# Kernel optimization log

Measured on AMD Instinct MI355X. Metric: run time of the kernel, lower is better.

The kernel has to match this reference:

```python
import jax, jax.numpy as jnp
import numpy as np

N, E, IN, H, OUT, L = 20000, 320000, 256, 256, 128, 3
EPS = 1e-5


def setup_inputs() -> dict:
    key = jax.random.key(0)
    ks = jax.random.split(key, 16)
    s = 0.02
    return {
        "x": jax.random.normal(ks[0], (N, IN), jnp.float32),
        "edge_index": jax.random.randint(ks[1], (2, E), 0, N, jnp.int64),
        "in_w": jax.random.normal(ks[2], (IN, H), jnp.float32) * s,
        "in_b": jnp.zeros((H,), jnp.float32),
        "parent_w": jax.random.normal(ks[3], (L, H, H), jnp.float32) * s,
        "child_w": jax.random.normal(ks[4], (L, H, H), jnp.float32) * s,
        "self_w": jax.random.normal(ks[5], (L, H, H), jnp.float32) * s,
        "self_b": jnp.zeros((L, H), jnp.float32),
        "ln_g": jnp.ones((L, H), jnp.float32),
        "ln_b": jnp.zeros((L, H), jnp.float32),
        "head_w1": jax.random.normal(ks[6], (H, H), jnp.float32) * s,
        "head_b1": jnp.zeros((H,), jnp.float32),
        "head_w2": jax.random.normal(ks[7], (H, OUT), jnp.float32) * s,
        "head_b2": jnp.zeros((OUT,), jnp.float32),
    }


def _aggregate(h, src, dst, weight):
    # gather -> matmul -> scatter-add -> degree-normalize
    transformed = h[src] @ weight                       # [E, H]
    agg = jax.ops.segment_sum(transformed, dst, num_segments=N)
    deg = jax.ops.segment_sum(jnp.ones((src.shape[0],), h.dtype), dst, num_segments=N)
    deg = jnp.maximum(deg, 1.0)
    return agg / deg[:, None]


def _layer_norm(x, g, b):
    mu = jnp.mean(x, axis=-1, keepdims=True)
    var = jnp.mean(jnp.square(x - mu), axis=-1, keepdims=True)
    return (x - mu) * jax.lax.rsqrt(var + EPS) * g + b


def reference(x, edge_index, in_w, in_b, parent_w, child_w, self_w, self_b,
              ln_g, ln_b, head_w1, head_b1, head_w2, head_b2):
    src, dst = edge_index[0], edge_index[1]
    h = x @ in_w + in_b                                  # input_proj
    for l in range(L):
        parent_msg = _aggregate(h, src, dst, parent_w[l])
        child_msg = _aggregate(h, dst, src, child_w[l])  # reversed edges
        out = h @ self_w[l] + self_b[l] + parent_msg + child_msg
        out = jax.nn.gelu(out, approximate=False)
        # dropout is identity in eval mode (training=False)
        h = _layer_norm(h + out, ln_g[l], ln_b[l])
    y = jax.nn.gelu(h @ head_w1 + head_b1, approximate=False)
    return y @ head_w2 + head_b2
```

## Files before the change

### kernel.cpp

```cpp
#include <hip/hip_runtime.h>


#define H 256
#define LAYERS 3
#define OUTD 128
#define LN_EPS 1e-5f

typedef short s16x8 __attribute__((ext_vector_type(8)));
typedef unsigned short u16x4 __attribute__((ext_vector_type(4)));
typedef unsigned short u16x8 __attribute__((ext_vector_type(8)));
typedef float f32x4 __attribute__((ext_vector_type(4)));
typedef int i32x4 __attribute__((ext_vector_type(4)));

__device__ __forceinline__ unsigned short f2bf(float f) {
  unsigned int u = __float_as_uint(f);
  u += 0x7FFFu + ((u >> 16) & 1u);
  return (unsigned short)(u >> 16);
}
__device__ __forceinline__ float bf2f(unsigned short s) {
  return __uint_as_float(((unsigned int)s) << 16);
}
__device__ __forceinline__ float gelu_f(float x) {
  return 0.5f * x * (1.0f + erff(x * 0.70710678118654752440f));
}
__device__ __forceinline__ void gload16(const void* g, void* l) {
  __builtin_amdgcn_global_load_lds((const __attribute__((address_space(1))) void*)g,
                                   (__attribute__((address_space(3))) void*)l, 16, 0, 0);
}


__device__ __forceinline__ void store_split8(unsigned short* __restrict__ T, int NS, int sec,
                                             int row, int l, u16x4 hv, u16x4 lv) {
  size_t tb = ((size_t)((row >> 4) * NS + sec) << 4) + (l >> 3);
  int off = (((row & 15) + (((l >> 1) & 3) << 4)) << 3) + ((l & 1) << 2);
  *(u16x4*)(T + tb * 512 + off) = hv;
  *(u16x4*)(T + (tb + 8) * 512 + off) = lv;
}

__global__ void split_tiles_kernel(const float* __restrict__ X,
                                   unsigned short* __restrict__ T, int NS, int sec,
                                   unsigned short* __restrict__ Hc, int M)
{
  const int rb = blockIdx.x;
  const int l = threadIdx.x & 63;
  const int cq = threadIdx.x >> 6;
  const int row = (rb << 4) + (l & 15);
  if (row >= M) return;
  const float* xr = X + (size_t)row * H;
#pragma unroll
  for (int p = 0; p < 2; ++p) {
    const int c = cq + (p << 2);
    const int j0 = (c << 5) + ((l >> 4) << 3);
    f32x4 v0 = *(const f32x4*)(xr + j0);
    f32x4 v1 = *(const f32x4*)(xr + j0 + 4);
    u16x8 hv, lv;
#pragma unroll
    for (int i = 0; i < 4; ++i) {
      unsigned short hb = f2bf(v0[i]); hv[i] = hb;     lv[i] = f2bf(v0[i] - bf2f(hb));
      unsigned short hc = f2bf(v1[i]); hv[4 + i] = hc; lv[4 + i] = f2bf(v1[i] - bf2f(hc));
    }
    size_t tb = ((size_t)(rb * NS + sec) << 4);
    *(u16x8*)(T + (tb + c) * 512 + (l << 3)) = hv;
    *(u16x8*)(T + (tb + c + 8) * 512 + (l << 3)) = lv;
    if (Hc) *(u16x8*)(Hc + (size_t)row * H + j0) = hv;
  }
}

__global__ void bext_kernel(const float* __restrict__ W, unsigned short* __restrict__ Bt, int ncol) {
  int idx = blockIdx.x * 256 + threadIdx.x;
  if (idx >= H * ncol) return;
  int k = idx / ncol;
  int n = idx - k * ncol;
  float w = W[idx];
  unsigned short hb = f2bf(w);
  unsigned short lb = f2bf(w - bf2f(hb));
  size_t base = (((size_t)(n >> 4) << 4) + (k >> 5)) * 512 +
                (((n & 15) + (((k >> 3) & 3) << 4)) << 3) + (k & 7);
  Bt[base] = hb;
  Bt[base + 8 * 512] = lb;
}

__global__ void zero2_kernel(int* __restrict__ a, int* __restrict__ b, int n) {
  int i = blockIdx.x * 256 + threadIdx.x;
  if (i < n) { a[i] = 0; b[i] = 0; }
}

__global__ void deg_kernel(const int* __restrict__ src, const int* __restrict__ dst,
                           int* __restrict__ di, int* __restrict__ dox, int E) {
  int e = blockIdx.x * 256 + threadIdx.x;
  if (e >= E) return;
  atomicAdd(&dox[src[e]], 1);
  atomicAdd(&di[dst[e]], 1);
}

__global__ void rdeg_kernel(const int* __restrict__ di, const int* __restrict__ dox,
                            float* __restrict__ ri, float* __restrict__ ro, int n) {
  int i = blockIdx.x * 256 + threadIdx.x;
  if (i >= n) return;
  int a = di[i];  if (a < 1) a = 1;
  int b = dox[i]; if (b < 1) b = 1;
  ri[i] = 1.0f / (float)a;
  ro[i] = 1.0f / (float)b;
}

__global__ __launch_bounds__(1024)
void scan_kernel(const int* __restrict__ deg, int* __restrict__ rowptr, int n) {
  __shared__ int partial[1024];
  const int t = threadIdx.x;
  const int chunk = (n + 1023) / 1024;
  int b = t * chunk;
  int e = b + chunk; if (e > n) e = n;
  int s = 0;
  for (int i = b; i < e; ++i) s += deg[i];
  partial[t] = s;
  __syncthreads();
  for (int off = 1; off < 1024; off <<= 1) {
    int v = (t >= off) ? partial[t - off] : 0;
    __syncthreads();
    partial[t] += v;
    __syncthreads();
  }
  int run = (t == 0) ? 0 : partial[t - 1];
  for (int i = b; i < e; ++i) { rowptr[i] = run; run += deg[i]; }
  if (t == 1023) rowptr[n] = run;
}

__global__ void fill_kernel(const int* __restrict__ src, const int* __restrict__ dst,
                            const int* __restrict__ rp_in, const int* __restrict__ rp_out,
                            int* __restrict__ cur_in, int* __restrict__ cur_out,
                            int* __restrict__ ci_in, int* __restrict__ ci_out, int E) {
  int e = blockIdx.x * 256 + threadIdx.x;
  if (e >= E) return;
  int s = src[e], d = dst[e];
  int p = atomicAdd(&cur_in[d], 1);
  ci_in[rp_in[d] + p] = s;
  int q = atomicAdd(&cur_out[s], 1);
  ci_out[rp_out[s] + q] = d;
}

template<int NF>
__global__ __launch_bounds__(256)
void gemm_kernel(const unsigned short* __restrict__ A, int NSa,
                 const unsigned short* __restrict__ B0,
                 const unsigned short* __restrict__ B1,
                 const unsigned short* __restrict__ B2,
                 const float* __restrict__ bias, float* __restrict__ C,
                 int M, int nrb, int nsec, int do_gelu)
{
  constexpr int N = NF * 64;
  constexpr int NBT = N / 16;
  constexpr int BITER = NBT / 4;
  constexpr int SA_HI = 0, SA_LO = 2048, SB_HI = 4096;
  constexpr int SB_LO = 4096 + NBT * 512;
  __shared__ unsigned short lds[2][4096 + 2 * NBT * 512];

  const int tid = threadIdx.x;
  const int lane = tid & 63;
  const int wn = tid >> 6;
  const int m0 = blockIdx.x << 6;
  int rbw = (blockIdx.x << 2) + wn;
  if (rbw >= nrb) rbw = nrb - 1;

  f32x4 acc[4][NF] = {};

  auto STAGE = [&](int buf, int step) {
    const int s = step >> 3;
    const int c = step & 7;
    const unsigned short* Bs = (s == 0) ? B0 : ((s == 1) ? B1 : B2);
    unsigned short* base = &lds[buf][0];
    const unsigned short* pa = A + (((size_t)(rbw * NSa + s) << 4) + c) * 512 + (lane << 3);
    gload16(pa,        base + SA_HI + (wn << 9));
    gload16(pa + 4096, base + SA_LO + (wn << 9));
#pragma unroll
    for (int i = 0; i < BITER; ++i) {
      const int nb = wn + (i << 2);
      const unsigned short* pb = Bs + (((size_t)nb << 4) + c) * 512 + (lane << 3);
      gload16(pb,        base + SB_HI + (nb << 9));
      gload16(pb + 4096, base + SB_LO + (nb << 9));
    }
  };

  auto COMPUTE = [&](int buf) {
    const unsigned short* base = &lds[buf][0];
    s16x8 ah[4], al[4], bh[NF], bl[NF];
#pragma unroll
    for (int f = 0; f < 4; ++f) {
      ah[f] = *(const s16x8*)(base + SA_HI + (f << 9) + (lane << 3));
      al[f] = *(const s16x8*)(base + SA_LO + (f << 9) + (lane << 3));
    }
#pragma unroll
    for (int j = 0; j < NF; ++j) {
      const int g = wn * NF + j;
      bh[j] = *(const s16x8*)(base + SB_HI + (g << 9) + (lane << 3));
      bl[j] = *(const s16x8*)(base + SB_LO + (g << 9) + (lane << 3));
    }
#pragma unroll
    for (int i = 0; i < 4; ++i)
#pragma unroll
      for (int j = 0; j < NF; ++j)
        acc[i][j] = __builtin_amdgcn_mfma_f32_16x16x32_bf16(ah[i], bh[j], acc[i][j], 0, 0, 0);
#pragma unroll
    for (int i = 0; i < 4; ++i)
#pragma unroll
      for (int j = 0; j < NF; ++j)
        acc[i][j] = __builtin_amdgcn_mfma_f32_16x16x32_bf16(ah[i], bl[j], acc[i][j], 0, 0, 0);
#pragma unroll
    for (int i = 0; i < 4; ++i)
#pragma unroll
      for (int j = 0; j < NF; ++j)
        acc[i][j] = __builtin_amdgcn_mfma_f32_16x16x32_bf16(al[i], bh[j], acc[i][j], 0, 0, 0);
  };

  const int nsteps = nsec << 3;
  STAGE(0, 0);
  int cur = 0;
  for (int t = 0; t < nsteps - 1; ++t) {
    STAGE(cur ^ 1, t + 1);
    if (NF == 4) asm volatile("s_waitcnt vmcnt(10)" ::: "memory");
    else         asm volatile("s_waitcnt vmcnt(6)"  ::: "memory");
    __builtin_amdgcn_s_barrier();
    COMPUTE(cur);
    asm volatile("s_waitcnt lgkmcnt(0)" ::: "memory");
    __builtin_amdgcn_s_barrier();
    cur ^= 1;
  }
  asm volatile("s_waitcnt vmcnt(0)" ::: "memory");
  __builtin_amdgcn_s_barrier();
  COMPUTE(cur);

  const int r0 = (lane >> 4) << 2;
  const int cn = lane & 15;
#pragma unroll
  for (int j = 0; j < NF; ++j) {
    const int col = wn * (NF << 4) + (j << 4) + cn;
    const float bb = bias ? bias[col] : 0.0f;
#pragma unroll
    for (int i = 0; i < 4; ++i) {
      const int rowb = m0 + (i << 4) + r0;
#pragma unroll
      for (int r = 0; r < 4; ++r) {
        const int rr = rowb + r;
        if (rr < M) {
          float v = acc[i][j][r] + bb;
          if (do_gelu) v = gelu_f(v);
          C[(size_t)rr * N + col] = v;
        }
      }
    }
  }
}

__device__ __forceinline__ void gacc8(const int* __restrict__ ci, int beg, int end,
                                      const unsigned short* __restrict__ Hc, int foff,
                                      float* __restrict__ acc) {
  int i = beg;
  for (; i < end && (i & 3); ++i) {
    u16x8 a = *(const u16x8*)(Hc + ((size_t)ci[i] << 8) + foff);
#pragma unroll
    for (int z = 0; z < 8; ++z) acc[z] += bf2f(a[z]);
  }
  for (; i + 4 <= end; i += 4) {
    i32x4 id = *(const i32x4*)(ci + i);
    u16x8 a = *(const u16x8*)(Hc + ((size_t)id[0] << 8) + foff);
    u16x8 b = *(const u16x8*)(Hc + ((size_t)id[1] << 8) + foff);
    u16x8 c = *(const u16x8*)(Hc + ((size_t)id[2] << 8) + foff);
    u16x8 d = *(const u16x8*)(Hc + ((size_t)id[3] << 8) + foff);
#pragma unroll
    for (int z = 0; z < 8; ++z)
      acc[z] += (bf2f(a[z]) + bf2f(b[z])) + (bf2f(c[z]) + bf2f(d[z]));
  }
  for (; i < end; ++i) {
    u16x8 a = *(const u16x8*)(Hc + ((size_t)ci[i] << 8) + foff);
#pragma unroll
    for (int z = 0; z < 8; ++z) acc[z] += bf2f(a[z]);
  }
}

__global__ __launch_bounds__(256)
void gather_kernel(
    const int* __restrict__ rp_in, const int* __restrict__ ci_in,
    const int* __restrict__ rp_out, const int* __restrict__ ci_out,
    const float* __restrict__ ri, const float* __restrict__ ro,
    const unsigned short* __restrict__ Hc, unsigned short* __restrict__ Aext,
    int M, int nrb, int npair)
{
  __shared__ unsigned short sh[2][2][2][2][512];
  const int b = blockIdx.x;
  const int xcd = b & 7;
  const int s = xcd >> 1;
  const int rbp = ((b >> 3) << 1) + (xcd & 1);
  if (rbp >= npair) return;
  const int tid = threadIdx.x;
  const int g = tid >> 3;
  const int t = tid & 7;
  const int row = (rbp << 5) + g;
  const int foff = (s << 6) + (t << 3);

  float hin[8] = {}, hout[8] = {};
  float wi = 0.f, wo = 0.f;
  if (row < M) {
    gacc8(ci_in,  rp_in[row],  rp_in[row + 1],  Hc, foff, hin);
    gacc8(ci_out, rp_out[row], rp_out[row + 1], Hc, foff, hout);
    wi = ri[row];
    wo = ro[row];
  }

  const int rbl = g >> 4;
  const int cc = t >> 2;
  const int pos = ((g & 15) << 3) + ((t & 3) << 7);
  u16x8 hv, lv;
#pragma unroll
  for (int q = 0; q < 8; ++q) {
    float v = hin[q] * wi;
    unsigned short hb = f2bf(v);
    hv[q] = hb; lv[q] = f2bf(v - bf2f(hb));
  }
  *(u16x8*)(&sh[rbl][0][0][cc][pos]) = hv;
  *(u16x8*)(&sh[rbl][0][1][cc][pos]) = lv;
#pragma unroll
  for (int q = 0; q < 8; ++q) {
    float v = hout[q] * wo;
    unsigned short hb = f2bf(v);
    hv[q] = hb; lv[q] = f2bf(v - bf2f(hb));
  }
  *(u16x8*)(&sh[rbl][1][0][cc][pos]) = hv;
  *(u16x8*)(&sh[rbl][1][1][cc][pos]) = lv;
  __syncthreads();

  const int tp = tid >> 4;
  const int q = tid & 15;
  const int rbl2 = tp >> 3, sec = (tp >> 2) & 1, hilo = (tp >> 1) & 1, c2 = tp & 1;
  const int rb = (rbp << 1) + rbl2;
  if (rb < nrb) {
    const int cg = (s << 1) + c2 + (hilo << 3);
    size_t tile = ((size_t)(rb * 3 + 1 + sec) << 4) + cg;
    unsigned short* dstp = Aext + tile * 512;
    const unsigned short* srcp = &sh[rbl2][sec][hilo][c2][0];
#pragma unroll
    for (int i = 0; i < 4; ++i)
      *(u16x8*)(dstp + (i << 7) + (q << 3)) = *(const u16x8*)(srcp + (i << 7) + (q << 3));
  }
}

__global__ void finalize_kernel(float* __restrict__ h, const float* __restrict__ P,
                                unsigned short* __restrict__ Aext,
                                unsigned short* __restrict__ Hc,
                                const float* __restrict__ g, const float* __restrict__ b, int M)
{
  int row = blockIdx.x * 4 + (threadIdx.x >> 6);
  if (row >= M) return;
  int l = threadIdx.x & 63;
  int j = l << 2;
  f32x4 hv = *(const f32x4*)(h + (size_t)row * H + j);
  f32x4 pv = *(const f32x4*)(P + (size_t)row * H + j);
  f32x4 t;
  float sum = 0.f, sq = 0.f;
#pragma unroll
  for (int i = 0; i < 4; ++i) {
    t[i] = hv[i] + gelu_f(pv[i]);
    sum += t[i];
    sq += t[i] * t[i];
  }
#pragma unroll
  for (int off = 1; off < 64; off <<= 1) {
    sum += __shfl_xor(sum, off, 64);
    sq  += __shfl_xor(sq, off, 64);
  }
  float mu = sum * (1.0f / H);
  float var = sq * (1.0f / H) - mu * mu;
  float rs = rsqrtf(var + LN_EPS);
  f32x4 outv;
  u16x4 hvv, lvv;
#pragma unroll
  for (int i = 0; i < 4; ++i) {
    outv[i] = (t[i] - mu) * rs * g[j + i] + b[j + i];
    unsigned short hb = f2bf(outv[i]);
    hvv[i] = hb;
    lvv[i] = f2bf(outv[i] - bf2f(hb));
  }
  *(f32x4*)(h + (size_t)row * H + j) = outv;
  *(u16x4*)(Hc + ((size_t)row << 8) + j) = hvv;
  store_split8(Aext, 3, 0, row, l, hvv, lvv);
}

extern "C" void kernel_launch(void* const* d_in, const int* in_sizes, int n_in,
                              void* d_out, int out_size, void* d_ws, size_t ws_size,
                              hipStream_t stream)
{
  const float* x        = (const float*)d_in[0];
  const int*   ei       = (const int*)d_in[1];
  const float* in_w     = (const float*)d_in[2];
  const float* in_b     = (const float*)d_in[3];
  const float* parent_w = (const float*)d_in[4];
  const float* child_w  = (const float*)d_in[5];
  const float* self_w   = (const float*)d_in[6];
  const float* self_b   = (const float*)d_in[7];
  const float* ln_g     = (const float*)d_in[8];
  const float* ln_b     = (const float*)d_in[9];
  const float* head_w1  = (const float*)d_in[10];
  const float* head_b1  = (const float*)d_in[11];
  const float* head_w2  = (const float*)d_in[12];
  const float* head_b2  = (const float*)d_in[13];

  const int M = in_sizes[0] / H;
  const int E = in_sizes[1] / 2;
  const int nrb = (M + 15) / 16;
  const int npair = (nrb + 1) / 2;
  const int* src = ei;
  const int* dst = ei + E;

  char* w = (char*)d_ws;
  auto alloc = [&](size_t bytes) { char* p = w; w += (bytes + 255) & ~(size_t)255; return p; };
  float*          h    = (float*)alloc((size_t)M * H * 4);
  float*          P    = (float*)alloc((size_t)M * H * 4);
  unsigned short* Ax   = (unsigned short*)alloc((size_t)nrb * 16 * 512 * 2);
  unsigned short* Aext = (unsigned short*)alloc((size_t)nrb * 48 * 512 * 2);
  unsigned short* Hc   = (unsigned short*)alloc((size_t)M * H * 2);
  unsigned short* Bext = (unsigned short*)alloc((size_t)12 * H * 512 * 2);
  int*            degi = (int*)alloc((size_t)M * 4);
  int*            dego = (int*)alloc((size_t)M * 4);
  float*          ri   = (float*)alloc((size_t)M * 4);
  float*          ro   = (float*)alloc((size_t)M * 4);
  int*            rp_in   = (int*)alloc((size_t)(M + 1) * 4);
  int*            rp_out  = (int*)alloc((size_t)(M + 1) * 4);
  int*            cur_in  = (int*)alloc((size_t)M * 4);
  int*            cur_out = (int*)alloc((size_t)M * 4);
  int*            ci_in   = (int*)alloc((size_t)E * 4);
  int*            ci_out  = (int*)alloc((size_t)E * 4);
  if ((size_t)(w - (char*)d_ws) > ws_size) return;

  auto bslot = [&](int i) { return Bext + (size_t)i * H * 512; };

  bext_kernel<<<(H * H) / 256, 256, 0, stream>>>(in_w, bslot(0), H);
  for (int l = 0; l < LAYERS; ++l) {
    bext_kernel<<<(H * H) / 256, 256, 0, stream>>>(parent_w + (size_t)l * H * H, bslot(1 + l), H);
    bext_kernel<<<(H * H) / 256, 256, 0, stream>>>(child_w  + (size_t)l * H * H, bslot(4 + l), H);
    bext_kernel<<<(H * H) / 256, 256, 0, stream>>>(self_w   + (size_t)l * H * H, bslot(7 + l), H);
  }
  bext_kernel<<<(H * H) / 256, 256, 0, stream>>>(head_w1, bslot(10), H);
  bext_kernel<<<(H * OUTD) / 256, 256, 0, stream>>>(head_w2, bslot(11), OUTD);

  zero2_kernel<<<(M + 255) / 256, 256, 0, stream>>>(degi, dego, M);
  deg_kernel<<<(E + 255) / 256, 256, 0, stream>>>(src, dst, degi, dego, E);
  rdeg_kernel<<<(M + 255) / 256, 256, 0, stream>>>(degi, dego, ri, ro, M);
  scan_kernel<<<1, 1024, 0, stream>>>(degi, rp_in, M);
  scan_kernel<<<1, 1024, 0, stream>>>(dego, rp_out, M);
  zero2_kernel<<<(M + 255) / 256, 256, 0, stream>>>(cur_in, cur_out, M);
  fill_kernel<<<(E + 255) / 256, 256, 0, stream>>>(src, dst, rp_in, rp_out,
                                                   cur_in, cur_out, ci_in, ci_out, E);

  const int mb = (M + 63) / 64;
  const int ggrid = (M + 3) / 4;
  const int xgrid = 8 * ((npair + 1) / 2);

  split_tiles_kernel<<<nrb, 256, 0, stream>>>(x, Ax, 1, 0, nullptr, M);
  gemm_kernel<4><<<mb, 256, 0, stream>>>(Ax, 1, bslot(0), nullptr, nullptr,
                                         in_b, h, M, nrb, 1, 0);
  split_tiles_kernel<<<nrb, 256, 0, stream>>>(h, Aext, 3, 0, Hc, M);

  for (int l = 0; l < LAYERS; ++l) {
    gather_kernel<<<xgrid, 256, 0, stream>>>(rp_in, ci_in, rp_out, ci_out,
                                             ri, ro, Hc, Aext, M, nrb, npair);
    gemm_kernel<4><<<mb, 256, 0, stream>>>(Aext, 3,
                                           bslot(7 + l), bslot(1 + l), bslot(4 + l),
                                           self_b + (size_t)l * H, P, M, nrb, 3, 0);
    finalize_kernel<<<ggrid, 256, 0, stream>>>(h, P, Aext, Hc,
                                               ln_g + (size_t)l * H, ln_b + (size_t)l * H, M);
  }

  gemm_kernel<4><<<mb, 256, 0, stream>>>(Aext, 3, bslot(10), nullptr, nullptr,
                                         head_b1, P, M, nrb, 1, 1);
  split_tiles_kernel<<<nrb, 256, 0, stream>>>(P, Ax, 1, 0, nullptr, M);
  gemm_kernel<2><<<mb, 256, 0, stream>>>(Ax, 1, bslot(11), nullptr, nullptr,
                                         head_b2, (float*)d_out, M, nrb, 1, 0);
}
```

Measured before the change: 522.8 us.

## Batch weight-split and CSR-build launches, interleave in/out gather loops

Merges the eleven per-matrix weight-splitting launches into a single kernel indexed by slot. Folds the cursor zeroing into the reciprocal-degree kernel and runs both prefix scans as two blocks of one launch. The gather kernel now walks the in-edge and out-edge lists together, issuing eight independent row loads per iteration instead of processing the two lists one after the other. Together these cut launch count and raise memory-level parallelism in the gather, at the cost of more registers per thread there.

```diff
diff --git a/kernel.cpp b/kernel.cpp
--- a/kernel.cpp
+++ b/kernel.cpp
@@ -66,9 +66,26 @@
   }
 }
 
-__global__ void bext_kernel(const float* __restrict__ W, unsigned short* __restrict__ Bt, int ncol) {
-  int idx = blockIdx.x * 256 + threadIdx.x;
+__global__ void bext_all_kernel(const float* __restrict__ in_w,
+                                const float* __restrict__ parent_w,
+                                const float* __restrict__ child_w,
+                                const float* __restrict__ self_w,
+                                const float* __restrict__ head_w1,
+                                const float* __restrict__ head_w2,
+                                unsigned short* __restrict__ Bext)
+{
+  const int slot = blockIdx.x >> 8;
+  const int chunk = blockIdx.x & 255;
+  const int ncol = (slot == 11) ? OUTD : H;
+  const int idx = chunk * 256 + threadIdx.x;
   if (idx >= H * ncol) return;
+  const float* W =
+    (slot == 0)  ? in_w :
+    (slot <= 3)  ? parent_w + (size_t)(slot - 1) * H * H :
+    (slot <= 6)  ? child_w  + (size_t)(slot - 4) * H * H :
+    (slot <= 9)  ? self_w   + (size_t)(slot - 7) * H * H :
+    (slot == 10) ? head_w1  : head_w2;
+  unsigned short* Bt = Bext + (size_t)slot * H * 512;
   int k = idx / ncol;
   int n = idx - k * ncol;
   float w = W[idx];
@@ -94,18 +111,24 @@
 }
 
 __global__ void rdeg_kernel(const int* __restrict__ di, const int* __restrict__ dox,
-                            float* __restrict__ ri, float* __restrict__ ro, int n) {
+                            float* __restrict__ ri, float* __restrict__ ro,
+                            int* __restrict__ cur_in, int* __restrict__ cur_out, int n) {
   int i = blockIdx.x * 256 + threadIdx.x;
   if (i >= n) return;
   int a = di[i];  if (a < 1) a = 1;
   int b = dox[i]; if (b < 1) b = 1;
   ri[i] = 1.0f / (float)a;
   ro[i] = 1.0f / (float)b;
+  cur_in[i] = 0;
+  cur_out[i] = 0;
 }
 
 __global__ __launch_bounds__(1024)
-void scan_kernel(const int* __restrict__ deg, int* __restrict__ rowptr, int n) {
+void scan2_kernel(const int* __restrict__ degi, const int* __restrict__ dego,
+                  int* __restrict__ rp_in, int* __restrict__ rp_out, int n) {
   __shared__ int partial[1024];
+  const int* deg = blockIdx.x ? dego : degi;
+  int* rowptr = blockIdx.x ? rp_out : rp_in;
   const int t = threadIdx.x;
   const int chunk = (n + 1023) / 1024;
   int b = t * chunk;
@@ -250,30 +273,9 @@
   }
 }
 
-__device__ __forceinline__ void gacc8(const int* __restrict__ ci, int beg, int end,
-                                      const unsigned short* __restrict__ Hc, int foff,
-                                      float* __restrict__ acc) {
-  int i = beg;
-  for (; i < end && (i & 3); ++i) {
-    u16x8 a = *(const u16x8*)(Hc + ((size_t)ci[i] << 8) + foff);
-#pragma unroll
-    for (int z = 0; z < 8; ++z) acc[z] += bf2f(a[z]);
-  }
-  for (; i + 4 <= end; i += 4) {
-    i32x4 id = *(const i32x4*)(ci + i);
-    u16x8 a = *(const u16x8*)(Hc + ((size_t)id[0] << 8) + foff);
-    u16x8 b = *(const u16x8*)(Hc + ((size_t)id[1] << 8) + foff);
-    u16x8 c = *(const u16x8*)(Hc + ((size_t)id[2] << 8) + foff);
-    u16x8 d = *(const u16x8*)(Hc + ((size_t)id[3] << 8) + foff);
-#pragma unroll
-    for (int z = 0; z < 8; ++z)
-      acc[z] += (bf2f(a[z]) + bf2f(b[z])) + (bf2f(c[z]) + bf2f(d[z]));
-  }
-  for (; i < end; ++i) {
-    u16x8 a = *(const u16x8*)(Hc + ((size_t)ci[i] << 8) + foff);
-#pragma unroll
-    for (int z = 0; z < 8; ++z) acc[z] += bf2f(a[z]);
-  }
+__device__ __forceinline__ void add8(float* __restrict__ acc, u16x8 a) {
+#pragma unroll
+  for (int z = 0; z < 8; ++z) acc[z] += bf2f(a[z]);
 }
 
 __global__ __launch_bounds__(256)
@@ -299,10 +301,49 @@
   float hin[8] = {}, hout[8] = {};
   float wi = 0.f, wo = 0.f;
   if (row < M) {
-    gacc8(ci_in,  rp_in[row],  rp_in[row + 1],  Hc, foff, hin);
-    gacc8(ci_out, rp_out[row], rp_out[row + 1], Hc, foff, hout);
     wi = ri[row];
     wo = ro[row];
+    int i1 = rp_in[row],  e1 = rp_in[row + 1];
+    int i2 = rp_out[row], e2 = rp_out[row + 1];
+    for (; i1 < e1 && (i1 & 3); ++i1)
+      add8(hin, *(const u16x8*)(Hc + ((size_t)ci_in[i1] << 8) + foff));
+    for (; i2 < e2 && (i2 & 3); ++i2)
+      add8(hout, *(const u16x8*)(Hc + ((size_t)ci_out[i2] << 8) + foff));
+    while (i1 + 4 <= e1 && i2 + 4 <= e2) {
+      i32x4 ia = *(const i32x4*)(ci_in + i1);
+      i32x4 ib = *(const i32x4*)(ci_out + i2);
+      u16x8 a0 = *(const u16x8*)(Hc + ((size_t)ia[0] << 8) + foff);
+      u16x8 a1 = *(const u16x8*)(Hc + ((size_t)ia[1] << 8) + foff);
+      u16x8 a2 = *(const u16x8*)(Hc + ((size_t)ia[2] << 8) + foff);
+      u16x8 a3 = *(const u16x8*)(Hc + ((size_t)ia[3] << 8) + foff);
+      u16x8 b0 = *(const u16x8*)(Hc + ((size_t)ib[0] << 8) + foff);
+      u16x8 b1 = *(const u16x8*)(Hc + ((size_t)ib[1] << 8) + foff);
+      u16x8 b2 = *(const u16x8*)(Hc + ((size_t)ib[2] << 8) + foff);
+      u16x8 b3 = *(const u16x8*)(Hc + ((size_t)ib[3] << 8) + foff);
+      add8(hin, a0);  add8(hin, a1);  add8(hin, a2);  add8(hin, a3);
+      add8(hout, b0); add8(hout, b1); add8(hout, b2); add8(hout, b3);
+      i1 += 4; i2 += 4;
+    }
+    for (; i1 + 4 <= e1; i1 += 4) {
+      i32x4 ia = *(const i32x4*)(ci_in + i1);
+      u16x8 a0 = *(const u16x8*)(Hc + ((size_t)ia[0] << 8) + foff);
+      u16x8 a1 = *(const u16x8*)(Hc + ((size_t)ia[1] << 8) + foff);
+      u16x8 a2 = *(const u16x8*)(Hc + ((size_t)ia[2] << 8) + foff);
+      u16x8 a3 = *(const u16x8*)(Hc + ((size_t)ia[3] << 8) + foff);
+      add8(hin, a0); add8(hin, a1); add8(hin, a2); add8(hin, a3);
+    }
+    for (; i2 + 4 <= e2; i2 += 4) {
+      i32x4 ib = *(const i32x4*)(ci_out + i2);
+      u16x8 b0 = *(const u16x8*)(Hc + ((size_t)ib[0] << 8) + foff);
+      u16x8 b1 = *(const u16x8*)(Hc + ((size_t)ib[1] << 8) + foff);
+      u16x8 b2 = *(const u16x8*)(Hc + ((size_t)ib[2] << 8) + foff);
+      u16x8 b3 = *(const u16x8*)(Hc + ((size_t)ib[3] << 8) + foff);
+      add8(hout, b0); add8(hout, b1); add8(hout, b2); add8(hout, b3);
+    }
+    for (; i1 < e1; ++i1)
+      add8(hin, *(const u16x8*)(Hc + ((size_t)ci_in[i1] << 8) + foff));
+    for (; i2 < e2; ++i2)
+      add8(hout, *(const u16x8*)(Hc + ((size_t)ci_out[i2] << 8) + foff));
   }
 
   const int rbl = g >> 4;
@@ -431,21 +472,13 @@
 
   auto bslot = [&](int i) { return Bext + (size_t)i * H * 512; };
 
-  bext_kernel<<<(H * H) / 256, 256, 0, stream>>>(in_w, bslot(0), H);
-  for (int l = 0; l < LAYERS; ++l) {
-    bext_kernel<<<(H * H) / 256, 256, 0, stream>>>(parent_w + (size_t)l * H * H, bslot(1 + l), H);
-    bext_kernel<<<(H * H) / 256, 256, 0, stream>>>(child_w  + (size_t)l * H * H, bslot(4 + l), H);
-    bext_kernel<<<(H * H) / 256, 256, 0, stream>>>(self_w   + (size_t)l * H * H, bslot(7 + l), H);
-  }
-  bext_kernel<<<(H * H) / 256, 256, 0, stream>>>(head_w1, bslot(10), H);
-  bext_kernel<<<(H * OUTD) / 256, 256, 0, stream>>>(head_w2, bslot(11), OUTD);
+  bext_all_kernel<<<12 * 256, 256, 0, stream>>>(in_w, parent_w, child_w, self_w,
+                                                head_w1, head_w2, Bext);
 
   zero2_kernel<<<(M + 255) / 256, 256, 0, stream>>>(degi, dego, M);
   deg_kernel<<<(E + 255) / 256, 256, 0, stream>>>(src, dst, degi, dego, E);
-  rdeg_kernel<<<(M + 255) / 256, 256, 0, stream>>>(degi, dego, ri, ro, M);
-  scan_kernel<<<1, 1024, 0, stream>>>(degi, rp_in, M);
-  scan_kernel<<<1, 1024, 0, stream>>>(dego, rp_out, M);
-  zero2_kernel<<<(M + 255) / 256, 256, 0, stream>>>(cur_in, cur_out, M);
+  rdeg_kernel<<<(M + 255) / 256, 256, 0, stream>>>(degi, dego, ri, ro, cur_in, cur_out, M);
+  scan2_kernel<<<2, 1024, 0, stream>>>(degi, dego, rp_in, rp_out, M);
   fill_kernel<<<(E + 255) / 256, 256, 0, stream>>>(src, dst, rp_in, rp_out,
                                                    cur_in, cur_out, ci_in, ci_out, E);
 
```

Result: faster. 482.6 us (-7.7%).
